# Performance work log

Measured on AMD Instinct MI355X. Metric: run time of the kernel, lower is better.

The kernel has to match this reference:

```python
import jax, jax.numpy as jnp
import numpy as np

EPS = 1e-8  # torch F.cosine_similarity denominator clamp


def setup_inputs() -> dict:
    key = jax.random.key(0)
    k1, k2, k3 = jax.random.split(key, 3)
    B, F, T = 64, 512, 600
    data_label = jax.random.randint(k1, (B, F, T), 0, 100, dtype=jnp.int64)
    feature_a = jax.random.normal(k2, (B, F, T), dtype=jnp.float32)
    feature_b = jax.random.normal(k3, (B, F, T), dtype=jnp.float32)
    return {"data_label": data_label, "feature_a": feature_a, "feature_b": feature_b}


def _merge(feat, seg, merge_size):
    # feat: [B, F, T] -> segment-sum over time -> [B, M, F]
    ft = jnp.moveaxis(feat, 2, 0)  # [T, B, F]
    merged = jax.ops.segment_sum(ft, seg, num_segments=merge_size)  # [M, B, F]
    return jnp.moveaxis(merged, 1, 0)  # [B, M, F]


def reference(data_label, feature_a, feature_b):
    B, F, T = feature_a.shape
    merge_size = (T - 1) // 3 + 1
    # Original: f_merge[(i_time-1)//3] += f[i_time]; Python floor-div gives -1
    # for t=0, i.e. timestep 0 lands in the LAST bucket (negative indexing).
    seg = jnp.floor_divide(jnp.arange(T) - 1, 3) % merge_size  # [T]

    fa = _merge(feature_a, seg, merge_size)  # [B, M, F]
    fb = _merge(feature_b, seg, merge_size)  # [B, M, F]

    # Pairwise cosine similarity: cos[b, i, j] = cos(fa[b,i], fb[b,j])
    num = jnp.einsum('bmf,bnf->bmn', fa, fb)
    na = jnp.linalg.norm(fa, axis=-1)  # [B, M]
    nb = jnp.linalg.norm(fb, axis=-1)  # [B, M]
    cos = num / jnp.maximum(na[:, :, None] * nb[:, None, :], EPS)  # [B, M, M]

    # criterion: cross-entropy with diagonal (matched-time) targets,
    # mean over M per batch element, summed over batch (loss += criterion(...)).
    logp = jax.nn.log_softmax(cos, axis=-1)  # [B, M, M]
    idx = jnp.arange(cos.shape[1])
    diag = logp[:, idx, idx]  # [B, M]
    loss = jnp.sum(-jnp.mean(diag, axis=-1))
    return loss
```

## Files before the change

kernel.cpp:

```cpp
#include <hip/hip_runtime.h>
#include <hip/hip_bf16.h>
#include <math.h>

#define B_ 64
#define F_ 512
#define T_ 600
#define M_ 200

typedef __attribute__((ext_vector_type(8))) short bf16x8_t;
typedef __attribute__((ext_vector_type(4))) float f32x4_t;

static __device__ __forceinline__ unsigned short f2bf(float v) {
    __hip_bfloat16 h = __float2bfloat16(v);
    return *reinterpret_cast<unsigned short*>(&h);
}
static __device__ __forceinline__ float bf2f(unsigned short u) {
    return __uint_as_float(((unsigned)u) << 16);
}

__global__ __launch_bounds__(320)
void merge_t_kernel(const float* __restrict__ a, const float* __restrict__ b,
                    unsigned short* __restrict__ fa, unsigned short* __restrict__ fb) {
    const float* src = (blockIdx.y == 0) ? a : b;
    unsigned short* dst = (blockIdx.y == 0) ? fa : fb;
    int blk = blockIdx.x;
    int bb  = blk >> 3;
    int f0  = (blk & 7) * 64;

    __shared__ unsigned short tile[64][210];

    int t = threadIdx.x;
    const float* rowbase = src + (size_t)(bb * F_ + f0) * T_;

    #pragma unroll 5
    for (int i = 0; i < 10; ++i) {
        int task = t + i * 320;
        int r = task / 50;
        int j = task - r * 50;
        const float4* rp = (const float4*)(rowbase + (size_t)r * T_);
        float4 q0 = rp[3 * j];
        float4 q1 = rp[3 * j + 1];
        float4 q2 = rp[3 * j + 2];
        float s0 = q0.y + q0.z + q0.w;
        float s1 = q1.x + q1.y + q1.z;
        float s2 = q1.w + q2.x + q2.y;
        float s3;
        if (j < 49) {
            float4 q3 = rp[3 * j + 3];
            s3 = q2.z + q2.w + q3.x;
        } else {
            s3 = ((const float*)rp)[0] + q2.z + q2.w;
        }
        ushort2 p01 = make_ushort2(f2bf(s0), f2bf(s1));
        ushort2 p23 = make_ushort2(f2bf(s2), f2bf(s3));
        *(ushort2*)&tile[r][4 * j]     = p01;
        *(ushort2*)&tile[r][4 * j + 2] = p23;
    }
    __syncthreads();

    int lane8 = t & 7;
    int grp   = t >> 3;
    #pragma unroll
    for (int it = 0; it < 5; ++it) {
        int m = grp + it * 40;
        union { unsigned short s[8]; uint4 q; } u;
        #pragma unroll
        for (int k = 0; k < 8; ++k) u.s[k] = tile[lane8 * 8 + k][m];
        *(uint4*)(dst + (size_t)(bb * M_ + m) * F_ + f0 + lane8 * 8) = u.q;
    }
}

__global__ __launch_bounds__(256)
void norm_kernel(const unsigned short* __restrict__ fa, const unsigned short* __restrict__ fb,
                 float* __restrict__ na, float* __restrict__ nb) {
    const unsigned short* src = (blockIdx.y == 0) ? fa : fb;
    float*                dst = (blockIdx.y == 0) ? na : nb;
    int wave = threadIdx.x >> 6;
    int lane = threadIdx.x & 63;
    int bm = blockIdx.x * 4 + wave;
    const ushort4* p = (const ushort4*)(src + (size_t)bm * F_ + lane * 8);
    ushort4 u0 = p[0], u1 = p[1];
    float acc = 0.f;
    float x;
    x = bf2f(u0.x); acc = fmaf(x, x, acc);
    x = bf2f(u0.y); acc = fmaf(x, x, acc);
    x = bf2f(u0.z); acc = fmaf(x, x, acc);
    x = bf2f(u0.w); acc = fmaf(x, x, acc);
    x = bf2f(u1.x); acc = fmaf(x, x, acc);
    x = bf2f(u1.y); acc = fmaf(x, x, acc);
    x = bf2f(u1.z); acc = fmaf(x, x, acc);
    x = bf2f(u1.w); acc = fmaf(x, x, acc);
    #pragma unroll
    for (int off = 32; off >= 1; off >>= 1)
        acc += __shfl_xor(acc, off, 64);
    if (lane == 0) dst[bm] = sqrtf(acc);
}

#define BK_ 64
__global__ __launch_bounds__(256)
void gemm_kernel(const unsigned short* __restrict__ fa, const unsigned short* __restrict__ fb,
                 float* __restrict__ num) {
    __shared__ unsigned short As[64][88];
    __shared__ unsigned short Bs[64][88];

    int bb = blockIdx.z;
    int m0 = blockIdx.x * 64;
    int n0 = blockIdx.y * 64;
    const unsigned short* A = fa + (size_t)bb * M_ * F_;
    const unsigned short* B = fb + (size_t)bb * M_ * F_;

    int t    = threadIdx.x;
    int lane = t & 63;
    int wid  = t >> 6;
    int wm32 = (wid >> 1) * 32;
    int wn32 = (wid & 1) * 32;

    int sr = t >> 3;
    int sc = (t & 7) * 8;

    f32x4_t acc[2][2];
    #pragma unroll
    for (int i = 0; i < 2; ++i)
        #pragma unroll
        for (int j = 0; j < 2; ++j)
            acc[i][j] = (f32x4_t)(0.f);

    const uint4 z4 = make_uint4(0, 0, 0, 0);
    for (int k0 = 0; k0 < F_; k0 += BK_) {
        #pragma unroll
        for (int p = 0; p < 2; ++p) {
            int r  = p * 32 + sr;
            int gm = m0 + r, gn = n0 + r;
            uint4 va = z4, vb = z4;
            if (gm < M_) va = *(const uint4*)(A + (size_t)gm * F_ + k0 + sc);
            if (gn < M_) vb = *(const uint4*)(B + (size_t)gn * F_ + k0 + sc);
            *(uint4*)&As[r][sc] = va;
            *(uint4*)&Bs[r][sc] = vb;
        }
        __syncthreads();
        #pragma unroll
        for (int kk = 0; kk < 2; ++kk) {
            int kc = kk * 32 + (lane >> 4) * 8;
            int rl = lane & 15;
            bf16x8_t a0 = *(const bf16x8_t*)&As[wm32 + rl][kc];
            bf16x8_t a1 = *(const bf16x8_t*)&As[wm32 + 16 + rl][kc];
            bf16x8_t b0 = *(const bf16x8_t*)&Bs[wn32 + rl][kc];
            bf16x8_t b1 = *(const bf16x8_t*)&Bs[wn32 + 16 + rl][kc];
            acc[0][0] = __builtin_amdgcn_mfma_f32_16x16x32_bf16(a0, b0, acc[0][0], 0, 0, 0);
            acc[0][1] = __builtin_amdgcn_mfma_f32_16x16x32_bf16(a0, b1, acc[0][1], 0, 0, 0);
            acc[1][0] = __builtin_amdgcn_mfma_f32_16x16x32_bf16(a1, b0, acc[1][0], 0, 0, 0);
            acc[1][1] = __builtin_amdgcn_mfma_f32_16x16x32_bf16(a1, b1, acc[1][1], 0, 0, 0);
        }
        __syncthreads();
    }

    float* C = num + (size_t)bb * M_ * M_;
    int r0 = (lane >> 4) * 4;
    int cc = lane & 15;
    #pragma unroll
    for (int i = 0; i < 2; ++i) {
        #pragma unroll
        for (int j = 0; j < 2; ++j) {
            #pragma unroll
            for (int r = 0; r < 4; ++r) {
                int m = m0 + wm32 + i * 16 + r0 + r;
                int n = n0 + wn32 + j * 16 + cc;
                if (m < M_ && n < M_) C[(size_t)m * M_ + n] = acc[i][j][r];
            }
        }
    }
}

__global__ __launch_bounds__(256)
void row_softmax_kernel(const float* __restrict__ num,
                        const float* __restrict__ na,
                        const float* __restrict__ nb,
                        float* __restrict__ partial) {
    int wave = threadIdx.x >> 6;
    int lane = threadIdx.x & 63;
    int bm = blockIdx.x * 4 + wave;
    int b  = bm / M_;
    int m  = bm - b * M_;
    const float* row = num + (size_t)b * M_ * M_ + (size_t)m * M_;
    const float* nbp = nb + b * M_;
    float nam = na[bm];

    float cosv[4];
    float mx = -INFINITY;
    #pragma unroll
    for (int r = 0; r < 4; ++r) {
        int n = lane + r * 64;
        float c = -INFINITY;
        if (n < M_) {
            float denom = fmaxf(nam * nbp[n], 1e-8f);
            c = row[n] / denom;
        }
        cosv[r] = c;
        mx = fmaxf(mx, c);
    }
    #pragma unroll
    for (int off = 32; off >= 1; off >>= 1)
        mx = fmaxf(mx, __shfl_xor(mx, off, 64));

    float s = 0.f, diag = 0.f;
    #pragma unroll
    for (int r = 0; r < 4; ++r) {
        int n = lane + r * 64;
        if (n < M_) {
            s += __expf(cosv[r] - mx);
            if (n == m) diag = cosv[r];
        }
    }
    #pragma unroll
    for (int off = 32; off >= 1; off >>= 1) {
        s    += __shfl_xor(s, off, 64);
        diag += __shfl_xor(diag, off, 64);
    }
    if (lane == 0) {
        float lse = mx + __logf(s);
        partial[bm] = -(diag - lse) / (float)M_;
    }
}

__global__ __launch_bounds__(256)
void final_reduce_kernel(const float* __restrict__ partial, float* __restrict__ out, int n) {
    __shared__ float sm[256];
    float acc = 0.f;
    for (int i = threadIdx.x; i < n; i += 256) acc += partial[i];
    sm[threadIdx.x] = acc;
    __syncthreads();
    #pragma unroll
    for (int st = 128; st > 0; st >>= 1) {
        if (threadIdx.x < st) sm[threadIdx.x] += sm[threadIdx.x + st];
        __syncthreads();
    }
    if (threadIdx.x == 0) out[0] = sm[0];
}

extern "C" void kernel_launch(void* const* d_in, const int* in_sizes, int n_in,
                              void* d_out, int out_size, void* d_ws, size_t ws_size,
                              hipStream_t stream) {
    const float* a_in = (const float*)d_in[1];
    const float* b_in = (const float*)d_in[2];

    const size_t merged_elems = (size_t)B_ * M_ * F_;
    unsigned short* fa = (unsigned short*)d_ws;
    unsigned short* fb = fa + merged_elems;
    float* num     = (float*)(fb + merged_elems);
    float* na      = num + (size_t)B_ * M_ * M_;
    float* nb      = na + B_ * M_;
    float* partial = nb + B_ * M_;

    merge_t_kernel<<<dim3(B_ * (F_ / 64), 2), 320, 0, stream>>>(a_in, b_in, fa, fb);
    norm_kernel<<<dim3(B_ * M_ / 4, 2), 256, 0, stream>>>(fa, fb, na, nb);
    gemm_kernel<<<dim3(4, 4, B_), 256, 0, stream>>>(fa, fb, num);
    row_softmax_kernel<<<dim3(B_ * M_ / 4), 256, 0, stream>>>(num, na, nb, partial);
    final_reduce_kernel<<<1, 256, 0, stream>>>(partial, (float*)d_out, B_ * M_);
}
```

Measured before the change: 253.1 us.

## Fuse norm, GEMM, softmax-CE and reduction into one kernel per row block

Replaces the separate norm, GEMM, row-softmax and final-reduce kernels with one kernel. Each block computes a 64-row stripe against all 200 columns of fb, accumulates squared norms while staging tiles, and computes cosine, log-softmax and the diagonal loss in registers. The loss is atomically added to the output, which the merge kernel zeroes. This removes the full similarity-matrix round trip and several launches. In exchange each block recomputes the fb norms, uses LDS atomics, has fewer blocks in flight, and makes the sum order nondeterministic.

Result: no change. 249.2 us (-1.5%).

```diff
diff --git a/kernel.cpp b/kernel.cpp
--- a/kernel.cpp
+++ b/kernel.cpp
@@ -6,6 +6,7 @@
 #define F_ 512
 #define T_ 600
 #define M_ 200
+#define NFRAG 13
 
 typedef __attribute__((ext_vector_type(8))) short bf16x8_t;
 typedef __attribute__((ext_vector_type(4))) float f32x4_t;
@@ -17,10 +18,20 @@
 static __device__ __forceinline__ float bf2f(unsigned short u) {
     return __uint_as_float(((unsigned)u) << 16);
 }
+static __device__ __forceinline__ float ssq8(uint4 v) {
+    const unsigned short* s = (const unsigned short*)&v;
+    float a = 0.f;
+    #pragma unroll
+    for (int i = 0; i < 8; ++i) { float x = bf2f(s[i]); a = fmaf(x, x, a); }
+    return a;
+}
 
 __global__ __launch_bounds__(320)
 void merge_t_kernel(const float* __restrict__ a, const float* __restrict__ b,
-                    unsigned short* __restrict__ fa, unsigned short* __restrict__ fb) {
+                    unsigned short* __restrict__ fa, unsigned short* __restrict__ fb,
+                    float* __restrict__ out) {
+    if (blockIdx.x == 0 && blockIdx.y == 0 && threadIdx.x == 0) out[0] = 0.f;
+
     const float* src = (blockIdx.y == 0) ? a : b;
     unsigned short* dst = (blockIdx.y == 0) ? fa : fb;
     int blk = blockIdx.x;
@@ -71,170 +82,146 @@
 }
 
 __global__ __launch_bounds__(256)
-void norm_kernel(const unsigned short* __restrict__ fa, const unsigned short* __restrict__ fb,
-                 float* __restrict__ na, float* __restrict__ nb) {
-    const unsigned short* src = (blockIdx.y == 0) ? fa : fb;
-    float*                dst = (blockIdx.y == 0) ? na : nb;
-    int wave = threadIdx.x >> 6;
-    int lane = threadIdx.x & 63;
-    int bm = blockIdx.x * 4 + wave;
-    const ushort4* p = (const ushort4*)(src + (size_t)bm * F_ + lane * 8);
-    ushort4 u0 = p[0], u1 = p[1];
-    float acc = 0.f;
-    float x;
-    x = bf2f(u0.x); acc = fmaf(x, x, acc);
-    x = bf2f(u0.y); acc = fmaf(x, x, acc);
-    x = bf2f(u0.z); acc = fmaf(x, x, acc);
-    x = bf2f(u0.w); acc = fmaf(x, x, acc);
-    x = bf2f(u1.x); acc = fmaf(x, x, acc);
-    x = bf2f(u1.y); acc = fmaf(x, x, acc);
-    x = bf2f(u1.z); acc = fmaf(x, x, acc);
-    x = bf2f(u1.w); acc = fmaf(x, x, acc);
-    #pragma unroll
-    for (int off = 32; off >= 1; off >>= 1)
-        acc += __shfl_xor(acc, off, 64);
-    if (lane == 0) dst[bm] = sqrtf(acc);
-}
-
-#define BK_ 64
-__global__ __launch_bounds__(256)
-void gemm_kernel(const unsigned short* __restrict__ fa, const unsigned short* __restrict__ fb,
-                 float* __restrict__ num) {
+void fused_loss_kernel(const unsigned short* __restrict__ fa,
+                       const unsigned short* __restrict__ fb,
+                       float* __restrict__ out) {
     __shared__ unsigned short As[64][88];
-    __shared__ unsigned short Bs[64][88];
-
-    int bb = blockIdx.z;
+    __shared__ unsigned short Bs[208][88];
+    __shared__ float na_sq[64];
+    __shared__ float nb_sq[208];
+    __shared__ float wloss[4];
+
+    int bb = blockIdx.y;
     int m0 = blockIdx.x * 64;
-    int n0 = blockIdx.y * 64;
-    const unsigned short* A = fa + (size_t)bb * M_ * F_;
-    const unsigned short* B = fb + (size_t)bb * M_ * F_;
+    const unsigned short* A  = fa + (size_t)bb * M_ * F_;
+    const unsigned short* Bp = fb + (size_t)bb * M_ * F_;
 
     int t    = threadIdx.x;
     int lane = t & 63;
-    int wid  = t >> 6;
-    int wm32 = (wid >> 1) * 32;
-    int wn32 = (wid & 1) * 32;
-
-    int sr = t >> 3;
-    int sc = (t & 7) * 8;
-
-    f32x4_t acc[2][2];
-    #pragma unroll
-    for (int i = 0; i < 2; ++i)
-        #pragma unroll
-        for (int j = 0; j < 2; ++j)
-            acc[i][j] = (f32x4_t)(0.f);
-
+    int wave = t >> 6;
+    int g    = lane >> 4;
+    int c    = lane & 15;
+
+    if (t < 64)  na_sq[t] = 0.f;
+    if (t < 208) nb_sq[t] = 0.f;
+    __syncthreads();
+
+    f32x4_t acc[NFRAG];
+    #pragma unroll
+    for (int f = 0; f < NFRAG; ++f) acc[f] = (f32x4_t)(0.f);
+
+    float assq0 = 0.f, assq1 = 0.f;
     const uint4 z4 = make_uint4(0, 0, 0, 0);
-    for (int k0 = 0; k0 < F_; k0 += BK_) {
-        #pragma unroll
-        for (int p = 0; p < 2; ++p) {
-            int r  = p * 32 + sr;
-            int gm = m0 + r, gn = n0 + r;
-            uint4 va = z4, vb = z4;
-            if (gm < M_) va = *(const uint4*)(A + (size_t)gm * F_ + k0 + sc);
-            if (gn < M_) vb = *(const uint4*)(B + (size_t)gn * F_ + k0 + sc);
-            *(uint4*)&As[r][sc] = va;
-            *(uint4*)&Bs[r][sc] = vb;
+
+    for (int k0 = 0; k0 < F_; k0 += 64) {
+        {
+            int ar0 = t >> 3, kq = t & 7;
+            int gm0 = m0 + ar0;
+            uint4 v0 = z4;
+            if (gm0 < M_) v0 = *(const uint4*)(A + (size_t)gm0 * F_ + k0 + kq * 8);
+            *(uint4*)&As[ar0][kq * 8] = v0;
+            assq0 += ssq8(v0);
+            int ar1 = ar0 + 32;
+            int gm1 = m0 + ar1;
+            uint4 v1 = z4;
+            if (gm1 < M_) v1 = *(const uint4*)(A + (size_t)gm1 * F_ + k0 + kq * 8);
+            *(uint4*)&As[ar1][kq * 8] = v1;
+            assq1 += ssq8(v1);
+        }
+        #pragma unroll
+        for (int i = 0; i < 7; ++i) {
+            int idx = t + (i << 8);
+            if (idx < 1664) {
+                int br = idx >> 3, kq = idx & 7;
+                uint4 v = z4;
+                if (br < M_) v = *(const uint4*)(Bp + (size_t)br * F_ + k0 + kq * 8);
+                *(uint4*)&Bs[br][kq * 8] = v;
+                if (br < M_) atomicAdd(&nb_sq[br], ssq8(v));
+            }
         }
         __syncthreads();
         #pragma unroll
         for (int kk = 0; kk < 2; ++kk) {
-            int kc = kk * 32 + (lane >> 4) * 8;
-            int rl = lane & 15;
-            bf16x8_t a0 = *(const bf16x8_t*)&As[wm32 + rl][kc];
-            bf16x8_t a1 = *(const bf16x8_t*)&As[wm32 + 16 + rl][kc];
-            bf16x8_t b0 = *(const bf16x8_t*)&Bs[wn32 + rl][kc];
-            bf16x8_t b1 = *(const bf16x8_t*)&Bs[wn32 + 16 + rl][kc];
-            acc[0][0] = __builtin_amdgcn_mfma_f32_16x16x32_bf16(a0, b0, acc[0][0], 0, 0, 0);
-            acc[0][1] = __builtin_amdgcn_mfma_f32_16x16x32_bf16(a0, b1, acc[0][1], 0, 0, 0);
-            acc[1][0] = __builtin_amdgcn_mfma_f32_16x16x32_bf16(a1, b0, acc[1][0], 0, 0, 0);
-            acc[1][1] = __builtin_amdgcn_mfma_f32_16x16x32_bf16(a1, b1, acc[1][1], 0, 0, 0);
+            int kc = kk * 32 + g * 8;
+            bf16x8_t af = *(const bf16x8_t*)&As[wave * 16 + c][kc];
+            #pragma unroll
+            for (int f = 0; f < NFRAG; ++f) {
+                bf16x8_t bfr = *(const bf16x8_t*)&Bs[f * 16 + c][kc];
+                acc[f] = __builtin_amdgcn_mfma_f32_16x16x32_bf16(af, bfr, acc[f], 0, 0, 0);
+            }
         }
         __syncthreads();
     }
 
-    float* C = num + (size_t)bb * M_ * M_;
-    int r0 = (lane >> 4) * 4;
-    int cc = lane & 15;
-    #pragma unroll
-    for (int i = 0; i < 2; ++i) {
-        #pragma unroll
-        for (int j = 0; j < 2; ++j) {
-            #pragma unroll
-            for (int r = 0; r < 4; ++r) {
-                int m = m0 + wm32 + i * 16 + r0 + r;
-                int n = n0 + wn32 + j * 16 + cc;
-                if (m < M_ && n < M_) C[(size_t)m * M_ + n] = acc[i][j][r];
-            }
-        }
-    }
-}
-
-__global__ __launch_bounds__(256)
-void row_softmax_kernel(const float* __restrict__ num,
-                        const float* __restrict__ na,
-                        const float* __restrict__ nb,
-                        float* __restrict__ partial) {
-    int wave = threadIdx.x >> 6;
-    int lane = threadIdx.x & 63;
-    int bm = blockIdx.x * 4 + wave;
-    int b  = bm / M_;
-    int m  = bm - b * M_;
-    const float* row = num + (size_t)b * M_ * M_ + (size_t)m * M_;
-    const float* nbp = nb + b * M_;
-    float nam = na[bm];
-
-    float cosv[4];
-    float mx = -INFINITY;
+    #pragma unroll
+    for (int off = 1; off <= 4; off <<= 1) {
+        assq0 += __shfl_xor(assq0, off, 64);
+        assq1 += __shfl_xor(assq1, off, 64);
+    }
+    if ((t & 7) == 0) {
+        na_sq[t >> 3]        = assq0;
+        na_sq[32 + (t >> 3)] = assq1;
+    }
+    __syncthreads();
+
+    int m0w = m0 + wave * 16;
+    float na_r[4];
+    #pragma unroll
+    for (int r = 0; r < 4; ++r) na_r[r] = sqrtf(na_sq[wave * 16 + g * 4 + r]);
+
+    float mx[4] = {-INFINITY, -INFINITY, -INFINITY, -INFINITY};
+    float diag_cos[4] = {0.f, 0.f, 0.f, 0.f};
+    int f_diag = m0w >> 4;
+
+    #pragma unroll
+    for (int f = 0; f < NFRAG; ++f) {
+        float nbv = sqrtf(nb_sq[f * 16 + c]);
+        int col = f * 16 + c;
+        bool colok = (col < M_);
+        #pragma unroll
+        for (int r = 0; r < 4; ++r) {
+            float denom = fmaxf(na_r[r] * nbv, 1e-8f);
+            float cv = acc[f][r] / denom;
+            int row = m0w + g * 4 + r;
+            if (f == f_diag && row < M_ && c == g * 4 + r) diag_cos[r] = cv;
+            cv = colok ? cv : -INFINITY;
+            acc[f][r] = cv;
+            mx[r] = fmaxf(mx[r], cv);
+        }
+    }
+    #pragma unroll
+    for (int off = 1; off <= 8; off <<= 1)
+        #pragma unroll
+        for (int r = 0; r < 4; ++r)
+            mx[r] = fmaxf(mx[r], __shfl_xor(mx[r], off, 64));
+
+    float sm[4] = {0.f, 0.f, 0.f, 0.f};
+    #pragma unroll
+    for (int f = 0; f < NFRAG; ++f)
+        #pragma unroll
+        for (int r = 0; r < 4; ++r)
+            sm[r] += __expf(acc[f][r] - mx[r]);
+    #pragma unroll
+    for (int off = 1; off <= 8; off <<= 1)
+        #pragma unroll
+        for (int r = 0; r < 4; ++r)
+            sm[r] += __shfl_xor(sm[r], off, 64);
+
+    float loss = 0.f;
     #pragma unroll
     for (int r = 0; r < 4; ++r) {
-        int n = lane + r * 64;
-        float c = -INFINITY;
-        if (n < M_) {
-            float denom = fmaxf(nam * nbp[n], 1e-8f);
-            c = row[n] / denom;
-        }
-        cosv[r] = c;
-        mx = fmaxf(mx, c);
-    }
-    #pragma unroll
-    for (int off = 32; off >= 1; off >>= 1)
-        mx = fmaxf(mx, __shfl_xor(mx, off, 64));
-
-    float s = 0.f, diag = 0.f;
-    #pragma unroll
-    for (int r = 0; r < 4; ++r) {
-        int n = lane + r * 64;
-        if (n < M_) {
-            s += __expf(cosv[r] - mx);
-            if (n == m) diag = cosv[r];
-        }
-    }
-    #pragma unroll
-    for (int off = 32; off >= 1; off >>= 1) {
-        s    += __shfl_xor(s, off, 64);
-        diag += __shfl_xor(diag, off, 64);
-    }
-    if (lane == 0) {
-        float lse = mx + __logf(s);
-        partial[bm] = -(diag - lse) / (float)M_;
-    }
-}
-
-__global__ __launch_bounds__(256)
-void final_reduce_kernel(const float* __restrict__ partial, float* __restrict__ out, int n) {
-    __shared__ float sm[256];
-    float acc = 0.f;
-    for (int i = threadIdx.x; i < n; i += 256) acc += partial[i];
-    sm[threadIdx.x] = acc;
-    __syncthreads();
-    #pragma unroll
-    for (int st = 128; st > 0; st >>= 1) {
-        if (threadIdx.x < st) sm[threadIdx.x] += sm[threadIdx.x + st];
-        __syncthreads();
-    }
-    if (threadIdx.x == 0) out[0] = sm[0];
+        int row = m0w + g * 4 + r;
+        if (row < M_ && c == g * 4 + r) {
+            float lse = mx[r] + __logf(sm[r]);
+            loss -= (diag_cos[r] - lse) * (1.0f / (float)M_);
+        }
+    }
+    #pragma unroll
+    for (int off = 1; off <= 32; off <<= 1)
+        loss += __shfl_xor(loss, off, 64);
+    if (lane == 0) wloss[wave] = loss;
+    __syncthreads();
+    if (t == 0) atomicAdd(out, wloss[0] + wloss[1] + wloss[2] + wloss[3]);
 }
 
 extern "C" void kernel_launch(void* const* d_in, const int* in_sizes, int n_in,
@@ -246,14 +233,8 @@
     const size_t merged_elems = (size_t)B_ * M_ * F_;
     unsigned short* fa = (unsigned short*)d_ws;
     unsigned short* fb = fa + merged_elems;
-    float* num     = (float*)(fb + merged_elems);
-    float* na      = num + (size_t)B_ * M_ * M_;
-    float* nb      = na + B_ * M_;
-    float* partial = nb + B_ * M_;
-
-    merge_t_kernel<<<dim3(B_ * (F_ / 64), 2), 320, 0, stream>>>(a_in, b_in, fa, fb);
-    norm_kernel<<<dim3(B_ * M_ / 4, 2), 256, 0, stream>>>(fa, fb, na, nb);
-    gemm_kernel<<<dim3(4, 4, B_), 256, 0, stream>>>(fa, fb, num);
-    row_softmax_kernel<<<dim3(B_ * M_ / 4), 256, 0, stream>>>(num, na, nb, partial);
-    final_reduce_kernel<<<1, 256, 0, stream>>>(partial, (float*)d_out, B_ * M_);
-}
+    float* out = (float*)d_out;
+
+    merge_t_kernel<<<dim3(B_ * (F_ / 64), 2), 320, 0, stream>>>(a_in, b_in, fa, fb, out);
+    fused_loss_kernel<<<dim3(4, B_), 256, 0, stream>>>(fa, fb, out);
+}
```
